# Kernel tuning notes

Hardware: AMD Instinct MI355X
Metric: run time of the kernel (lower is better)

Reference implementation:

```python
import jax, jax.numpy as jnp
import numpy as np

N_CAT, N_NUM, N_EMB, N_ENG = 53, 47, 1352, 100
E, H, FF, NEXP, NL = 128, 4, 256, 5, 6
B, L = 512, 51
EPS = 1e-5

def _ln(x, w, b):
    m = jnp.mean(x, axis=-1, keepdims=True)
    v = jnp.mean((x - m) ** 2, axis=-1, keepdims=True)
    return (x - m) * jax.lax.rsqrt(v + EPS) * w + b

def setup_inputs() -> dict:
    key = jax.random.key(0)
    ks = jax.random.split(key, 24)
    s = 0.02
    emb = jax.random.normal(ks[0], (N_EMB + 2, E), jnp.float32) * s
    emb = emb.at[0].set(0.0)  # padding_idx=0
    emb_eng = jax.random.normal(ks[1], (N_ENG, E), jnp.float32) * s
    emb_eng = emb_eng.at[0].set(0.0)
    inp = {
        'x_cat': jax.random.randint(ks[2], (B, L, N_CAT), 0, 1306, jnp.int32),
        'x_num': jax.random.normal(ks[3], (B, L, N_NUM), jnp.float32),
        'x_engineered': jax.random.normal(ks[4], (B, N_ENG), jnp.float32),
        'emb': emb,
        'emb_bias': jax.random.normal(ks[5], (N_CAT + N_NUM, E), jnp.float32),
        'emb_eng': emb_eng,
        'emb_bias_eng': jax.random.normal(ks[6], (N_ENG, E), jnp.float32),
        'ln0_w': jnp.ones((E,), jnp.float32), 'ln0_b': jnp.zeros((E,), jnp.float32),
        'ln1_w': jnp.ones((NL, E), jnp.float32), 'ln1_b': jnp.zeros((NL, E), jnp.float32),
        'Wqkv': jax.random.normal(ks[7], (NL, 3 * E, E), jnp.float32) * s,
        'bqkv': jnp.zeros((NL, 3 * E), jnp.float32),
        'Wo': jax.random.normal(ks[8], (NL, E, E), jnp.float32) * s,
        'bo': jnp.zeros((NL, E), jnp.float32),
        'ln2_w': jnp.ones((NL, E), jnp.float32), 'ln2_b': jnp.zeros((NL, E), jnp.float32),
        'Wg': jax.random.normal(ks[9], (NL, E, NEXP), jnp.float32) * s,
        'bg': jnp.zeros((NL, NEXP), jnp.float32),
        'W1': jax.random.normal(ks[10], (NL, NEXP, E, FF), jnp.float32) * s,
        'b1': jnp.zeros((NL, NEXP, FF), jnp.float32),
        'W2': jax.random.normal(ks[11], (NL, NEXP, FF, E), jnp.float32) * s,
        'b2': jnp.zeros((NL, NEXP, E), jnp.float32),
    }
    return inp

def _forward(x_cat, x_num, x_engineered, emb, emb_bias, emb_eng, emb_bias_eng,
             ln0_w, ln0_b, ln1_w, ln1_b, Wqkv, bqkv, Wo, bo,
             ln2_w, ln2_b, Wg, bg, W1, b1, W2, b2):
    b = x_cat.shape[0]
    # last order
    cat_last = x_cat[:, -1, :]                     # [B, N_CAT]
    num_last = x_num[:, -1, :]                     # [B, N_NUM]
    x_cat_emb = emb[cat_last] + emb_bias[:N_CAT][None]          # [B, N_CAT, E]
    num_idx = jnp.arange(N_EMB - N_NUM + 1, N_EMB + 1)           # rows 1306..1352
    x_num_emb = emb[num_idx][None] * num_last[..., None] + emb_bias[N_CAT:][None]
    eng_emb = emb_eng[None] * x_engineered[..., None] + emb_bias_eng[None]
    dummy = jnp.zeros((b, 1, E), x_cat_emb.dtype)
    x = jnp.concatenate([x_cat_emb, x_num_emb, eng_emb, dummy], axis=1)  # [B, 201, E]
    x = _ln(x, ln0_w, ln0_b)
    hd = E // H
    scale = 1.0 / np.sqrt(hd)
    for i in range(NL):
        # pre-norm multi-head self-attention
        h = _ln(x, ln1_w[i], ln1_b[i])
        qkv = h @ Wqkv[i].T + bqkv[i]              # [B, N, 3E]
        q, k, v = jnp.split(qkv, 3, axis=-1)
        q = q.reshape(b, -1, H, hd); k = k.reshape(b, -1, H, hd); v = v.reshape(b, -1, H, hd)
        scores = jnp.einsum('bqhd,bkhd->bhqk', q, k) * scale
        attn = jax.nn.softmax(scores, axis=-1)
        o = jnp.einsum('bhqk,bkhd->bqhd', attn, v).reshape(b, -1, E)
        x = x + o @ Wo[i].T + bo[i]
        # pre-norm MoE feedforward (dense soft mixture over experts)
        h = _ln(x, ln2_w[i], ln2_b[i])
        gate = jax.nn.softmax(h @ Wg[i] + bg[i], axis=-1)        # [B, N, NEXP]
        hid = jax.nn.relu(jnp.einsum('bne,xef->bnxf', h, W1[i]) + b1[i])
        eo = jnp.einsum('bnxf,xfe->bnxe', hid, W2[i]) + b2[i]
        x = x + jnp.einsum('bnxe,bnx->bne', eo, gate)
    return x[:, -1, :]                              # [B, E]

def reference(x_cat, x_num, x_engineered, emb, emb_bias, emb_eng, emb_bias_eng,
              ln0_w, ln0_b, ln1_w, ln1_b, Wqkv, bqkv, Wo, bo,
              ln2_w, ln2_b, Wg, bg, W1, b1, W2, b2):
    return _forward(x_cat, x_num, x_engineered, emb, emb_bias, emb_eng, emb_bias_eng,
                    ln0_w, ln0_b, ln1_w, ln1_b, Wqkv, bqkv, Wo, bo,
                    ln2_w, ln2_b, Wg, bg, W1, b1, W2, b2)
```

## Files before the change

### kernel.cpp

```cpp
#include <hip/hip_runtime.h>
#include <math.h>

#define NTOK 201
#define EDIM 128
#define LDX  132
#define NHEAD 4
#define HD   32
#define NLAY 6
#define NEXP 5
#define FFD  256
#define NCAT 53
#define NNUM 47
#define NENG 100
#define NEMB 1352
#define SEQL 51
#define NB   512
#define LN_EPS 1e-5f
#define SCALE 0.17677669529663687f

typedef __attribute__((ext_vector_type(8))) short bfrag;
typedef __attribute__((ext_vector_type(4))) float f32x4;
typedef __attribute__((ext_vector_type(8))) unsigned short u16x8;
typedef __attribute__((ext_vector_type(4))) unsigned short u16x4;

__device__ __forceinline__ float bf2f(unsigned short u){ return __uint_as_float(((unsigned)u)<<16); }
__device__ __forceinline__ unsigned short f2bf(float f){
  unsigned u = __float_as_uint(f);
  return (unsigned short)((u + 0x7FFFu + ((u>>16)&1u)) >> 16);
}

#define OFF_WQH  0u
#define OFF_WQL  589824u
#define OFF_BQ   1179648u
#define OFF_WOH  1188864u
#define OFF_WOL  1385472u
#define OFF_W1H  1582080u
#define OFF_W1L  3548160u
#define OFF_W2H  5514240u
#define OFF_W2L  7480320u

__global__ void prep_qkv_bf(const float* __restrict__ Wqkv, const float* __restrict__ bqkv,
                            unsigned short* __restrict__ Wqh, unsigned short* __restrict__ Wql,
                            float* __restrict__ bq){
  int bid = blockIdx.x; int n = bid % 384; int e = threadIdx.x;
  float sc = (n < 128) ? SCALE : 1.0f;
  float w = Wqkv[(size_t)bid*128 + e] * sc;
  unsigned short h = f2bf(w), l = f2bf(w - bf2f(h));
  Wqh[(size_t)bid*128 + e] = h; Wql[(size_t)bid*128 + e] = l;
  if (e == 0) bq[bid] = bqkv[bid] * sc;
}

__global__ void prep_wo_bf(const float* __restrict__ Wo,
                           unsigned short* __restrict__ Woh, unsigned short* __restrict__ Wol){
  int idx = blockIdx.x*blockDim.x + threadIdx.x;
  if (idx >= 6*128*128) return;
  float w = Wo[idx];
  unsigned short h = f2bf(w), l = f2bf(w - bf2f(h));
  Woh[idx] = h; Wol[idx] = l;
}

__global__ void prep_moe(const float* __restrict__ W1, const float* __restrict__ W2,
                         unsigned short* __restrict__ W1h, unsigned short* __restrict__ W1l,
                         unsigned short* __restrict__ W2h, unsigned short* __restrict__ W2l){
  const int Ntot = 6*5*128*256;
  for (int idx = blockIdx.x*blockDim.x + threadIdx.x; idx < Ntot; idx += gridDim.x*blockDim.x){
    int lx = idx / 32768; int rem = idx & 32767; int e = rem >> 8; int f = rem & 255;
    float w = W1[idx];
    unsigned short h = f2bf(w); unsigned short l = f2bf(w - bf2f(h));
    size_t o1 = (size_t)(lx*256+f)*128 + e;
    W1h[o1] = h; W1l[o1] = l;
    int f2 = (idx >> 7) & 255; int e2 = idx & 127;
    float w2 = W2[idx];
    unsigned short h2 = f2bf(w2); unsigned short l2 = f2bf(w2 - bf2f(h2));
    size_t o2 = (size_t)(lx*128+e2)*256 + f2;
    W2h[o2] = h2; W2l[o2] = l2;
  }
}

struct Params {
  const int*   x_cat;
  const float* x_num;
  const float* x_eng;
  const float* emb;
  const float* emb_bias;
  const float* emb_eng;
  const float* emb_bias_eng;
  const float* ln0w; const float* ln0b;
  const float* ln1w; const float* ln1b;
  const float* ln2w; const float* ln2b;
  const float* bo;
  const float* Wg;   const float* bg;
  const float* b1;   const float* b2;
  const unsigned short* Wqh; const unsigned short* Wql; const float* bq;
  const unsigned short* Woh; const unsigned short* Wol;
  const unsigned short* W1h; const unsigned short* W1l;
  const unsigned short* W2h; const unsigned short* W2l;
  float* out;
};

__device__ __forceinline__ void ln_stats(const float* xs, float* s_m, float* s_r, int tid){
  if (tid < NTOK){
    const float* row = xs + tid*LDX;
    float s0=0,s1=0,s2=0,s3=0;
    for (int e=0;e<EDIM;e+=4){ s0+=row[e]; s1+=row[e+1]; s2+=row[e+2]; s3+=row[e+3]; }
    float m = (s0+s1+s2+s3)*(1.0f/EDIM);
    float v0=0,v1=0,v2=0,v3=0;
    for (int e=0;e<EDIM;e+=4){
      float d0=row[e]-m,d1=row[e+1]-m,d2=row[e+2]-m,d3=row[e+3]-m;
      v0+=d0*d0; v1+=d1*d1; v2+=d2*d2; v3+=d3*d3;
    }
    s_m[tid]=m; s_r[tid]=1.0f/sqrtf((v0+v1+v2+v3)*(1.0f/EDIM)+LN_EPS);
  }
}

__global__ __launch_bounds__(512) __attribute__((amdgpu_waves_per_eu(2,2)))
void fam_fwd(Params p){
  __shared__ float xs[NTOK*LDX];
  __shared__ float s_m[NTOK], s_r[NTOK];
  __shared__ __align__(16) char scb[55296];

  const int b = blockIdx.x, tid = threadIdx.x;
  const int lane = tid & 63, wv = tid >> 6;

  {
    const int e = tid & 127, tl = tid >> 7;
    for (int t = tl; t < NTOK; t += 4){
      float v;
      if (t < NCAT){
        int idx = p.x_cat[b*(SEQL*NCAT) + (SEQL-1)*NCAT + t];
        v = p.emb[idx*EDIM+e] + p.emb_bias[t*EDIM+e];
      } else if (t < NCAT+NNUM){
        int j = t - NCAT;
        float nv = p.x_num[b*(SEQL*NNUM)+(SEQL-1)*NNUM+j];
        v = p.emb[(NEMB-NNUM+1+j)*EDIM+e]*nv + p.emb_bias[(NCAT+j)*EDIM+e];
      } else if (t < NCAT+NNUM+NENG){
        int j = t - (NCAT+NNUM);
        float ev = p.x_eng[b*NENG+j];
        v = p.emb_eng[j*EDIM+e]*ev + p.emb_bias_eng[j*EDIM+e];
      } else v = 0.f;
      xs[t*LDX+e] = v;
    }
  }
  __syncthreads();
  ln_stats(xs, s_m, s_r, tid);
  __syncthreads();
  {
    const int e = tid & 127, tl = tid >> 7;
    for (int t = tl; t < NTOK; t += 4){
      float m = s_m[t], r = s_r[t];
      xs[t*LDX+e] = (xs[t*LDX+e]-m)*r*p.ln0w[e] + p.ln0b[e];
    }
  }
  __syncthreads();

  unsigned short* Kh  = (unsigned short*)scb;
  unsigned short* Vt  = (unsigned short*)(scb + 17920);
  unsigned short* HTh = (unsigned short*)(scb + 32768);
  unsigned short* HTl = (unsigned short*)(scb + 32768 + 8704);
  unsigned short* Sb  = (unsigned short*)(scb + 32768);
  unsigned short* Ob  = (unsigned short*)(scb + 32768 + 14848);
  unsigned short* Qmh = (unsigned short*)(scb + 50176);
  unsigned short* Qml = (unsigned short*)(scb + 52736);
  float* red  = (float*)(scb + 52736);
  float* mrow = (float*)(scb + 52736 + 1056);
  float* dsum = (float*)(scb + 52736 + 1184);
  unsigned short* Ahi = (unsigned short*)scb;
  unsigned short* Alo = (unsigned short*)(scb + 8192);
  unsigned short* Hh  = (unsigned short*)(scb + 16384);
  unsigned short* Hl  = (unsigned short*)(scb + 32768);
  float*          gateb = (float*)(scb + 49152);

  for (int li = 0; li < NLAY; ++li){
    const float* ln1w = p.ln1w + li*EDIM;
    const float* ln1b = p.ln1b + li*EDIM;
    const float* ln2w = p.ln2w + li*EDIM;
    const float* ln2b = p.ln2b + li*EDIM;
    const float* bo   = p.bo + li*EDIM;
    const float* Wg   = p.Wg + li*EDIM*NEXP;
    const float* bg   = p.bg + li*NEXP;
    const float* b1g  = p.b1 + li*NEXP*FFD;
    const float* b2g  = p.b2 + li*NEXP*EDIM;

    ln_stats(xs, s_m, s_r, tid);
    __syncthreads();

    f32x4 accW[7][2];
#pragma unroll
    for (int mt=0; mt<7; ++mt){ accW[mt][0]=(f32x4){0,0,0,0}; accW[mt][1]=(f32x4){0,0,0,0}; }

    const int mfw = wv & 1;
    const int ngw = wv >> 1;

    for (int h = 0; h < NHEAD; ++h){
      {
        int sel = ngw;
        int nrow = ((sel < 2) ? (128 + h*HD + sel*16) : (256 + h*HD + (sel-2)*16)) + (lane & 15);
        const unsigned short* Bh = p.Wqh + ((size_t)li*384 + nrow)*128 + 8*(lane>>4);
        const unsigned short* Bl = p.Wql + ((size_t)li*384 + nrow)*128 + 8*(lane>>4);
        bfrag wbh[4], wbl[4];
#pragma unroll
        for (int kf=0; kf<4; ++kf){ wbh[kf] = *(const bfrag*)(Bh + kf*32); wbl[kf] = *(const bfrag*)(Bl + kf*32); }
        float bias = p.bq[li*384 + nrow];

        for (int mt=0; mt<7; ++mt){
          {
            int row = tid >> 4, c8 = (tid & 15) << 3;
            int t = mt*32 + row;
            union { unsigned short u[8]; u16x8 v; } hu, lu;
            if (t < NTOK){
              float m = s_m[t], r = s_r[t];
              const float* xr = &xs[t*LDX + c8];
              float4 a = *(const float4*)xr, b4 = *(const float4*)(xr+4);
              float4 w0 = *(const float4*)(ln1w + c8), w1 = *(const float4*)(ln1w + c8 + 4);
              float4 q0 = *(const float4*)(ln1b + c8), q1 = *(const float4*)(ln1b + c8 + 4);
              float vv[8] = {(a.x-m)*r*w0.x+q0.x,(a.y-m)*r*w0.y+q0.y,(a.z-m)*r*w0.z+q0.z,(a.w-m)*r*w0.w+q0.w,
                             (b4.x-m)*r*w1.x+q1.x,(b4.y-m)*r*w1.y+q1.y,(b4.z-m)*r*w1.z+q1.z,(b4.w-m)*r*w1.w+q1.w};
#pragma unroll
              for (int j2=0;j2<8;++j2){ unsigned short hb=f2bf(vv[j2]); hu.u[j2]=hb; lu.u[j2]=f2bf(vv[j2]-bf2f(hb)); }
            } else {
#pragma unroll
              for (int j2=0;j2<8;++j2){ hu.u[j2]=0; lu.u[j2]=0; }
            }
            *(u16x8*)(HTh + row*136 + c8) = hu.v;
            *(u16x8*)(HTl + row*136 + c8) = lu.v;
          }
          __syncthreads();
          {
            f32x4 acc = (f32x4){0,0,0,0};
#pragma unroll
            for (int kf=0; kf<4; ++kf){
              const unsigned short* ab = HTh + (mfw*16 + (lane&15))*136 + kf*32 + 8*(lane>>4);
              const unsigned short* al = HTl + (mfw*16 + (lane&15))*136 + kf*32 + 8*(lane>>4);
              bfrag ah = *(const bfrag*)ab, av = *(const bfrag*)al;
              acc = __builtin_amdgcn_mfma_f32_16x16x32_bf16(ah, wbh[kf], acc, 0,0,0);
              acc = __builtin_amdgcn_mfma_f32_16x16x32_bf16(ah, wbl[kf], acc, 0,0,0);
              acc = __builtin_amdgcn_mfma_f32_16x16x32_bf16(av, wbh[kf], acc, 0,0,0);
            }
            int col = lane & 15;
            if (sel < 2){
              int d = sel*16 + col;
#pragma unroll
              for (int reg=0; reg<4; ++reg){
                int tok = mt*32 + mfw*16 + 4*(lane>>4) + reg;
                Kh[tok*40 + d] = f2bf(acc[reg] + bias);
              }
            } else {
              int d = (sel-2)*16 + col;
              int tokb = mt*32 + mfw*16 + 4*(lane>>4);
              u16x4 pk;
#pragma unroll
              for (int reg=0; reg<4; ++reg) pk[reg] = f2bf(acc[reg] + bias);
              *(u16x4*)(Vt + d*232 + tokb) = pk;
            }
          }
          __syncthreads();
        }
      }

      bfrag wobh[2], wobl[2];
#pragma unroll
      for (int i=0;i<2;++i){
        int j = (ngw + 4*i)*16 + (lane&15);
        const unsigned short* wb = p.Woh + ((size_t)li*128 + j)*128 + h*HD + 8*(lane>>4);
        const unsigned short* wl = p.Wol + ((size_t)li*128 + j)*128 + h*HD + 8*(lane>>4);
        wobh[i] = *(const bfrag*)wb; wobl[i] = *(const bfrag*)wl;
      }

#pragma unroll
      for (int mt=0; mt<7; ++mt){
        {
          int row = tid >> 4, c8 = (tid & 15) << 3;
          int t = mt*32 + row;
          union { unsigned short u[8]; u16x8 v; } hu, lu;
          if (t < NTOK){
            float m = s_m[t], r = s_r[t];
            const float* xr = &xs[t*LDX + c8];
            float4 a = *(const float4*)xr, b4 = *(const float4*)(xr+4);
            float4 w0 = *(const float4*)(ln1w + c8), w1 = *(const float4*)(ln1w + c8 + 4);
            float4 q0 = *(const float4*)(ln1b + c8), q1 = *(const float4*)(ln1b + c8 + 4);
            float vv[8] = {(a.x-m)*r*w0.x+q0.x,(a.y-m)*r*w0.y+q0.y,(a.z-m)*r*w0.z+q0.z,(a.w-m)*r*w0.w+q0.w,
                           (b4.x-m)*r*w1.x+q1.x,(b4.y-m)*r*w1.y+q1.y,(b4.z-m)*r*w1.z+q1.z,(b4.w-m)*r*w1.w+q1.w};
#pragma unroll
            for (int j2=0;j2<8;++j2){ unsigned short hb=f2bf(vv[j2]); hu.u[j2]=hb; lu.u[j2]=f2bf(vv[j2]-bf2f(hb)); }
          } else {
#pragma unroll
            for (int j2=0;j2<8;++j2){ hu.u[j2]=0; lu.u[j2]=0; }
          }
          *(u16x8*)(HTh + row*136 + c8) = hu.v;
          *(u16x8*)(HTl + row*136 + c8) = lu.v;
        }
        __syncthreads();

        if (wv < 4){
          int mf2 = wv & 1, nf = (wv >> 1) & 1;
          int nrow = h*HD + nf*16 + (lane & 15);
          const unsigned short* Bh = p.Wqh + ((size_t)li*384 + nrow)*128 + 8*(lane>>4);
          const unsigned short* Bl = p.Wql + ((size_t)li*384 + nrow)*128 + 8*(lane>>4);
          f32x4 acc = (f32x4){0,0,0,0};
#pragma unroll
          for (int kf=0; kf<4; ++kf){
            bfrag ah = *(const bfrag*)(HTh + (mf2*16 + (lane&15))*136 + kf*32 + 8*(lane>>4));
            bfrag av = *(const bfrag*)(HTl + (mf2*16 + (lane&15))*136 + kf*32 + 8*(lane>>4));
            bfrag bh = *(const bfrag*)(Bh + kf*32);
            bfrag bl = *(const bfrag*)(Bl + kf*32);
            acc = __builtin_amdgcn_mfma_f32_16x16x32_bf16(ah, bh, acc, 0,0,0);
            acc = __builtin_amdgcn_mfma_f32_16x16x32_bf16(ah, bl, acc, 0,0,0);
            acc = __builtin_amdgcn_mfma_f32_16x16x32_bf16(av, bh, acc, 0,0,0);
          }
          float bias = p.bq[li*384 + nrow];
          int d = nf*16 + (lane & 15);
#pragma unroll
          for (int reg=0; reg<4; ++reg){
            float v = acc[reg] + bias;
            unsigned short hb = f2bf(v);
            int qrow = mf2*16 + 4*(lane>>4) + reg;
            Qmh[qrow*40 + d] = hb;
            Qml[qrow*40 + d] = f2bf(v - bf2f(hb));
          }
        }
        __syncthreads();

        {
          bfrag qh = *(const bfrag*)(Qmh + (mfw*16 + (lane&15))*40 + 8*(lane>>4));
          bfrag ql = *(const bfrag*)(Qml + (mfw*16 + (lane&15))*40 + 8*(lane>>4));
          for (int nf = ngw; nf < 14; nf += 4){
            bfrag kb = *(const bfrag*)(Kh + (nf*16 + (lane&15))*40 + 8*(lane>>4));
            f32x4 s = (f32x4){0,0,0,0};
            s = __builtin_amdgcn_mfma_f32_16x16x32_bf16(qh, kb, s, 0,0,0);
            s = __builtin_amdgcn_mfma_f32_16x16x32_bf16(ql, kb, s, 0,0,0);
            int tok = nf*16 + (lane & 15);
#pragma unroll
            for (int reg=0; reg<4; ++reg){
              int q = mfw*16 + 4*(lane>>4) + reg;
              Sb[q*232 + tok] = f2bf(s[reg]);
            }
          }
        }
        __syncthreads();

        {
          int q = tid & 31, kg = tid >> 5;
          float pmax = -INFINITY;
#pragma unroll
          for (int j2=0; j2<14; ++j2){
            int k = kg + 16*j2;
            if (k < NTOK) pmax = fmaxf(pmax, bf2f(Sb[q*232 + k]));
          }
          pmax = fmaxf(pmax, __shfl_xor(pmax, 32));
          if (!(tid & 32)) red[(tid>>6)*33 + q] = pmax;
        }
        __syncthreads();
        if (tid < 32){
          float m = red[tid];
#pragma unroll
          for (int w=1; w<8; ++w) m = fmaxf(m, red[w*33 + tid]);
          mrow[tid] = m;
        }
        __syncthreads();

        {
          int q = tid & 31, kg = tid >> 5;
          float mr = mrow[q];
          float psum = 0.f;
#pragma unroll
          for (int j2=0; j2<14; ++j2){
            int k = kg + 16*j2;
            float pe = 0.f;
            if (k < NTOK) pe = __expf(bf2f(Sb[q*232 + k]) - mr);
            psum += pe;
            Sb[q*232 + k] = f2bf(pe);
          }
          psum += __shfl_xor(psum, 32);
          if (!(tid & 32)) red[(tid>>6)*33 + q] = psum;
        }
        __syncthreads();
        if (tid < 32){
          float s = red[tid];
#pragma unroll
          for (int w=1; w<8; ++w) s += red[w*33 + tid];
          dsum[tid] = s;
        }
        __syncthreads();

        if (wv < 4){
          int mf2 = wv & 1, nf = (wv >> 1) & 1;
          f32x4 o = (f32x4){0,0,0,0};
#pragma unroll
          for (int kf=0; kf<7; ++kf){
            bfrag pa = *(const bfrag*)(Sb + (mf2*16 + (lane&15))*232 + kf*32 + 8*(lane>>4));
            bfrag vb = *(const bfrag*)(Vt + (nf*16 + (lane&15))*232 + kf*32 + 8*(lane>>4));
            o = __builtin_amdgcn_mfma_f32_16x16x32_bf16(pa, vb, o, 0,0,0);
          }
          int d = nf*16 + (lane & 15);
#pragma unroll
          for (int reg=0; reg<4; ++reg){
            int q = mf2*16 + 4*(lane>>4) + reg;
            Ob[q*40 + d] = f2bf(o[reg] * (1.0f/dsum[q]));
          }
        }
        __syncthreads();

        {
          bfrag oa = *(const bfrag*)(Ob + (mfw*16 + (lane&15))*40 + 8*(lane>>4));
          accW[mt][0] = __builtin_amdgcn_mfma_f32_16x16x32_bf16(oa, wobh[0], accW[mt][0], 0,0,0);
          accW[mt][0] = __builtin_amdgcn_mfma_f32_16x16x32_bf16(oa, wobl[0], accW[mt][0], 0,0,0);
          accW[mt][1] = __builtin_amdgcn_mfma_f32_16x16x32_bf16(oa, wobh[1], accW[mt][1], 0,0,0);
          accW[mt][1] = __builtin_amdgcn_mfma_f32_16x16x32_bf16(oa, wobl[1], accW[mt][1], 0,0,0);
        }
        __syncthreads();
      }
    }

    {
#pragma unroll
      for (int i=0;i<2;++i){
        int j = (ngw + 4*i)*16 + (lane & 15);
        float boj = bo[j];
#pragma unroll
        for (int mt=0; mt<7; ++mt){
#pragma unroll
          for (int reg=0; reg<4; ++reg){
            int t = mt*32 + mfw*16 + 4*(lane>>4) + reg;
            if (t < NTOK) xs[t*LDX + j] += accW[mt][i][reg] + boj;
          }
        }
      }
    }
    __syncthreads();

    ln_stats(xs, s_m, s_r, tid);
    __syncthreads();

    if (tid < NTOK){
      const float* row = xs + tid*LDX;
      float m = s_m[tid], r = s_r[tid];
      float gl[NEXP];
#pragma unroll
      for (int x=0;x<NEXP;++x) gl[x] = bg[x];
      for (int e=0;e<EDIM;++e){
        float hv = (row[e]-m)*r*ln2w[e] + ln2b[e];
#pragma unroll
        for (int x=0;x<NEXP;++x) gl[x] += hv*Wg[e*NEXP+x];
      }
      float gm = gl[0];
#pragma unroll
      for (int x=1;x<NEXP;++x) gm = fmaxf(gm, gl[x]);
      float gs = 0.f;
#pragma unroll
      for (int x=0;x<NEXP;++x){ gl[x] = __expf(gl[x]-gm); gs += gl[x]; }
      float gi = 1.0f/gs;
#pragma unroll
      for (int x=0;x<NEXP;++x) gateb[tid*NEXP+x] = gl[x]*gi;
    }
    __syncthreads();

    for (int t0 = 0; t0 < NTOK; t0 += 32){
      {
        int mf = tid >> 8;
        int row = (tid & 15) + 16*mf;
        int kb  = ((tid>>6)&3)*32 + 8*((tid>>4)&3);
        int t = t0 + row;
        union { unsigned short u[8]; bfrag v; } hu, lu;
        if (t < NTOK){
          float m = s_m[t], r = s_r[t];
          const float* xr = &xs[t*LDX + kb];
          float4 a = *(const float4*)xr;
          float4 bq4 = *(const float4*)(xr+4);
          float4 w0 = *(const float4*)(ln2w + kb);
          float4 w1 = *(const float4*)(ln2w + kb + 4);
          float4 bb0 = *(const float4*)(ln2b + kb);
          float4 bb1 = *(const float4*)(ln2b + kb + 4);
          float vv[8] = {(a.x-m)*r*w0.x+bb0.x, (a.y-m)*r*w0.y+bb0.y,
                         (a.z-m)*r*w0.z+bb0.z, (a.w-m)*r*w0.w+bb0.w,
                         (bq4.x-m)*r*w1.x+bb1.x, (bq4.y-m)*r*w1.y+bb1.y,
                         (bq4.z-m)*r*w1.z+bb1.z, (bq4.w-m)*r*w1.w+bb1.w};
#pragma unroll
          for (int j=0;j<8;++j){
            unsigned short hb = f2bf(vv[j]);
            hu.u[j] = hb;
            lu.u[j] = f2bf(vv[j] - bf2f(hb));
          }
        } else {
#pragma unroll
          for (int j=0;j<8;++j){ hu.u[j]=0; lu.u[j]=0; }
        }
        *(bfrag*)(Ahi + tid*8) = hu.v;
        *(bfrag*)(Alo + tid*8) = lu.v;
      }
      __syncthreads();

      f32x4 acc2[2];
      acc2[0] = (f32x4){0.f,0.f,0.f,0.f};
      acc2[1] = (f32x4){0.f,0.f,0.f,0.f};

      for (int x = 0; x < NEXP; ++x){
        const unsigned short* W1hx = p.W1h + (size_t)(li*NEXP+x)*FFD*EDIM;
        const unsigned short* W1lx = p.W1l + (size_t)(li*NEXP+x)*FFD*EDIM;
        const unsigned short* W2hx = p.W2h + (size_t)(li*NEXP+x)*EDIM*FFD;
        const unsigned short* W2lx = p.W2l + (size_t)(li*NEXP+x)*EDIM*FFD;

        f32x4 acc1[2][2];
#pragma unroll
        for (int i=0;i<2;++i){ acc1[i][0]=(f32x4){0,0,0,0}; acc1[i][1]=(f32x4){0,0,0,0}; }
#pragma unroll
        for (int kf=0;kf<4;++kf){
          bfrag ah[2], al[2], bh[2], bl[2];
#pragma unroll
          for (int mf=0;mf<2;++mf){
            ah[mf] = *(const bfrag*)(Ahi + ((mf*4+kf)*64 + lane)*8);
            al[mf] = *(const bfrag*)(Alo + ((mf*4+kf)*64 + lane)*8);
          }
#pragma unroll
          for (int nfl=0;nfl<2;++nfl){
            size_t n = (size_t)((wv*2+nfl)*16 + (lane&15));
            size_t off = n*128 + kf*32 + 8*(lane>>4);
            bh[nfl] = *(const bfrag*)(W1hx + off);
            bl[nfl] = *(const bfrag*)(W1lx + off);
          }
#pragma unroll
          for (int mf=0;mf<2;++mf)
#pragma unroll
            for (int nfl=0;nfl<2;++nfl){
              acc1[mf][nfl] = __builtin_amdgcn_mfma_f32_16x16x32_bf16(ah[mf], bh[nfl], acc1[mf][nfl], 0,0,0);
              acc1[mf][nfl] = __builtin_amdgcn_mfma_f32_16x16x32_bf16(ah[mf], bl[nfl], acc1[mf][nfl], 0,0,0);
              acc1[mf][nfl] = __builtin_amdgcn_mfma_f32_16x16x32_bf16(al[mf], bh[nfl], acc1[mf][nfl], 0,0,0);
            }
        }
        {
          int c = lane & 15;
#pragma unroll
          for (int nfl=0;nfl<2;++nfl){
            int n = (wv*2+nfl)*16 + c;
            float bb = b1g[x*FFD + n];
            int lane_t_base = 16*(2*nfl + (c>>3));
            int jcol = c & 7;
#pragma unroll
            for (int mf=0;mf<2;++mf){
#pragma unroll
              for (int reg=0;reg<4;++reg){
                int msub = (lane>>4)*4 + reg;
                int t = t0 + mf*16 + msub;
                float g = (t < NTOK) ? gateb[t*NEXP+x] : 0.f;
                float v = fmaxf(acc1[mf][nfl][reg] + bb, 0.f) * g;
                unsigned short hb = f2bf(v);
                unsigned short lb = f2bf(v - bf2f(hb));
                int idx = ((mf*8 + wv)*64 + msub + lane_t_base)*8 + jcol;
                Hh[idx] = hb; Hl[idx] = lb;
              }
            }
          }
        }
        __syncthreads();

#pragma unroll
        for (int kf=0;kf<8;++kf){
          bfrag hh[2], hl[2];
#pragma unroll
          for (int mf=0;mf<2;++mf){
            hh[mf] = *(const bfrag*)(Hh + ((mf*8+kf)*64 + lane)*8);
            hl[mf] = *(const bfrag*)(Hl + ((mf*8+kf)*64 + lane)*8);
          }
          size_t off = (size_t)(wv*16 + (lane&15))*256 + kf*32 + 8*(lane>>4);
          bfrag wh = *(const bfrag*)(W2hx + off);
          bfrag wl = *(const bfrag*)(W2lx + off);
#pragma unroll
          for (int mf=0;mf<2;++mf){
            acc2[mf] = __builtin_amdgcn_mfma_f32_16x16x32_bf16(hh[mf], wh, acc2[mf], 0,0,0);
            acc2[mf] = __builtin_amdgcn_mfma_f32_16x16x32_bf16(hh[mf], wl, acc2[mf], 0,0,0);
            acc2[mf] = __builtin_amdgcn_mfma_f32_16x16x32_bf16(hl[mf], wh, acc2[mf], 0,0,0);
          }
        }
        __syncthreads();
      }

      {
        int c = lane & 15;
        int n = wv*16 + c;
#pragma unroll
        for (int mf=0;mf<2;++mf){
#pragma unroll
          for (int reg=0;reg<4;++reg){
            int t = t0 + mf*16 + (lane>>4)*4 + reg;
            if (t < NTOK){
              float bs = 0.f;
#pragma unroll
              for (int x=0;x<NEXP;++x) bs += gateb[t*NEXP+x]*b2g[x*EDIM+n];
              xs[t*LDX+n] += acc2[mf][reg] + bs;
            }
          }
        }
      }
      __syncthreads();
    }
  }

  if (tid < EDIM) p.out[b*EDIM + tid] = xs[200*LDX + tid];
}

extern "C" void kernel_launch(void* const* d_in, const int* in_sizes, int n_in,
                              void* d_out, int out_size, void* d_ws, size_t ws_size,
                              hipStream_t stream) {
  (void)in_sizes; (void)n_in; (void)out_size; (void)ws_size;
  char* ws = (char*)d_ws;

  const float* Wqkv = (const float*)d_in[11];
  const float* bqkv = (const float*)d_in[12];
  const float* Wo   = (const float*)d_in[13];
  const float* W1   = (const float*)d_in[19];
  const float* W2   = (const float*)d_in[21];

  hipLaunchKernelGGL(prep_qkv_bf, dim3(6*384), dim3(128), 0, stream,
                     Wqkv, bqkv,
                     (unsigned short*)(ws+OFF_WQH), (unsigned short*)(ws+OFF_WQL),
                     (float*)(ws+OFF_BQ));
  hipLaunchKernelGGL(prep_wo_bf, dim3(384), dim3(256), 0, stream, Wo,
                     (unsigned short*)(ws+OFF_WOH), (unsigned short*)(ws+OFF_WOL));
  hipLaunchKernelGGL(prep_moe, dim3(3840), dim3(256), 0, stream, W1, W2,
                     (unsigned short*)(ws+OFF_W1H), (unsigned short*)(ws+OFF_W1L),
                     (unsigned short*)(ws+OFF_W2H), (unsigned short*)(ws+OFF_W2L));

  Params p;
  p.x_cat        = (const int*)  d_in[0];
  p.x_num        = (const float*)d_in[1];
  p.x_eng        = (const float*)d_in[2];
  p.emb          = (const float*)d_in[3];
  p.emb_bias     = (const float*)d_in[4];
  p.emb_eng      = (const float*)d_in[5];
  p.emb_bias_eng = (const float*)d_in[6];
  p.ln0w = (const float*)d_in[7];  p.ln0b = (const float*)d_in[8];
  p.ln1w = (const float*)d_in[9];  p.ln1b = (const float*)d_in[10];
  p.ln2w = (const float*)d_in[15]; p.ln2b = (const float*)d_in[16];
  p.bo   = (const float*)d_in[14];
  p.Wg   = (const float*)d_in[17]; p.bg = (const float*)d_in[18];
  p.b1   = (const float*)d_in[20]; p.b2 = (const float*)d_in[22];
  p.Wqh = (const unsigned short*)(ws+OFF_WQH);
  p.Wql = (const unsigned short*)(ws+OFF_WQL);
  p.bq  = (const float*)(ws+OFF_BQ);
  p.Woh = (const unsigned short*)(ws+OFF_WOH);
  p.Wol = (const unsigned short*)(ws+OFF_WOL);
  p.W1h = (const unsigned short*)(ws+OFF_W1H);
  p.W1l = (const unsigned short*)(ws+OFF_W1L);
  p.W2h = (const unsigned short*)(ws+OFF_W2H);
  p.W2l = (const unsigned short*)(ws+OFF_W2L);
  p.out = (float*)d_out;

  hipLaunchKernelGGL(fam_fwd, dim3(NB), dim3(512), 0, stream, p);
}
```

Measured before the change: 5.539 ms.

## Fuse softmax max into score pass, double-buffer MoE hidden, split accumulators

The row-max reduction for softmax now happens in registers via shuffles during the QK^T pass, and the sum reduction is folded into the PV epilogue, which drops several block barriers. In the MoE FFN, the hidden activation is double-buffered across experts so the barrier after each W2 pass can be removed. The hidden is also kept as a single bf16 term rather than a hi/lo split, which cuts one MFMA per step at some precision cost. The diff further splits MFMA accumulator chains to shorten dependencies, adds s_setprio around MFMA loops, and moves one barrier out of the inner loop.

```diff
diff --git a/kernel.cpp b/kernel.cpp
--- a/kernel.cpp
+++ b/kernel.cpp
@@ -111,6 +111,31 @@
     }
     s_m[tid]=m; s_r[tid]=1.0f/sqrtf((v0+v1+v2+v3)*(1.0f/EDIM)+LN_EPS);
   }
+}
+
+__device__ __forceinline__ void stage_ht(const float* xs, const float* s_m, const float* s_r,
+                                         unsigned short* HTh, unsigned short* HTl,
+                                         const float* lw, const float* lb, int t0, int tid){
+  int row = tid >> 4;
+  int c8  = (tid & 15) << 3;
+  int t = t0 + row;
+  union { unsigned short u[8]; u16x8 v; } hu, lu;
+  if (t < NTOK){
+    float m = s_m[t], r = s_r[t];
+    const float* xr = &xs[t*LDX + c8];
+    float4 a = *(const float4*)xr, b4 = *(const float4*)(xr+4);
+    float4 w0 = *(const float4*)(lw + c8), w1 = *(const float4*)(lw + c8 + 4);
+    float4 q0 = *(const float4*)(lb + c8), q1 = *(const float4*)(lb + c8 + 4);
+    float vv[8] = {(a.x-m)*r*w0.x+q0.x,(a.y-m)*r*w0.y+q0.y,(a.z-m)*r*w0.z+q0.z,(a.w-m)*r*w0.w+q0.w,
+                   (b4.x-m)*r*w1.x+q1.x,(b4.y-m)*r*w1.y+q1.y,(b4.z-m)*r*w1.z+q1.z,(b4.w-m)*r*w1.w+q1.w};
+#pragma unroll
+    for (int j2=0;j2<8;++j2){ unsigned short hb=f2bf(vv[j2]); hu.u[j2]=hb; lu.u[j2]=f2bf(vv[j2]-bf2f(hb)); }
+  } else {
+#pragma unroll
+    for (int j2=0;j2<8;++j2){ hu.u[j2]=0; lu.u[j2]=0; }
+  }
+  *(u16x8*)(HTh + row*136 + c8) = hu.v;
+  *(u16x8*)(HTl + row*136 + c8) = lu.v;
 }
 
 __global__ __launch_bounds__(512) __attribute__((amdgpu_waves_per_eu(2,2)))
@@ -162,12 +187,11 @@
   unsigned short* Qmh = (unsigned short*)(scb + 50176);
   unsigned short* Qml = (unsigned short*)(scb + 52736);
   float* red  = (float*)(scb + 52736);
-  float* mrow = (float*)(scb + 52736 + 1056);
-  float* dsum = (float*)(scb + 52736 + 1184);
+  float* red2 = (float*)(scb + 50176);
   unsigned short* Ahi = (unsigned short*)scb;
   unsigned short* Alo = (unsigned short*)(scb + 8192);
-  unsigned short* Hh  = (unsigned short*)(scb + 16384);
-  unsigned short* Hl  = (unsigned short*)(scb + 32768);
+  unsigned short* H0  = (unsigned short*)(scb + 16384);
+  unsigned short* H1  = (unsigned short*)(scb + 32768);
   float*          gateb = (float*)(scb + 49152);
 
   for (int li = 0; li < NLAY; ++li){
@@ -200,56 +224,42 @@
         bfrag wbh[4], wbl[4];
 #pragma unroll
         for (int kf=0; kf<4; ++kf){ wbh[kf] = *(const bfrag*)(Bh + kf*32); wbl[kf] = *(const bfrag*)(Bl + kf*32); }
-        float bias = p.bq[li*384 + nrow];
+        float bias1 = p.bq[li*384 + nrow];
 
         for (int mt=0; mt<7; ++mt){
-          {
-            int row = tid >> 4, c8 = (tid & 15) << 3;
-            int t = mt*32 + row;
-            union { unsigned short u[8]; u16x8 v; } hu, lu;
-            if (t < NTOK){
-              float m = s_m[t], r = s_r[t];
-              const float* xr = &xs[t*LDX + c8];
-              float4 a = *(const float4*)xr, b4 = *(const float4*)(xr+4);
-              float4 w0 = *(const float4*)(ln1w + c8), w1 = *(const float4*)(ln1w + c8 + 4);
-              float4 q0 = *(const float4*)(ln1b + c8), q1 = *(const float4*)(ln1b + c8 + 4);
-              float vv[8] = {(a.x-m)*r*w0.x+q0.x,(a.y-m)*r*w0.y+q0.y,(a.z-m)*r*w0.z+q0.z,(a.w-m)*r*w0.w+q0.w,
-                             (b4.x-m)*r*w1.x+q1.x,(b4.y-m)*r*w1.y+q1.y,(b4.z-m)*r*w1.z+q1.z,(b4.w-m)*r*w1.w+q1.w};
-#pragma unroll
-              for (int j2=0;j2<8;++j2){ unsigned short hb=f2bf(vv[j2]); hu.u[j2]=hb; lu.u[j2]=f2bf(vv[j2]-bf2f(hb)); }
-            } else {
-#pragma unroll
-              for (int j2=0;j2<8;++j2){ hu.u[j2]=0; lu.u[j2]=0; }
-            }
-            *(u16x8*)(HTh + row*136 + c8) = hu.v;
-            *(u16x8*)(HTl + row*136 + c8) = lu.v;
-          }
+          stage_ht(xs, s_m, s_r, HTh, HTl, ln1w, ln1b, mt*32, tid);
           __syncthreads();
           {
-            f32x4 acc = (f32x4){0,0,0,0};
+            f32x4 aA = (f32x4){0,0,0,0}, aB = (f32x4){0,0,0,0};
 #pragma unroll
             for (int kf=0; kf<4; ++kf){
-              const unsigned short* ab = HTh + (mfw*16 + (lane&15))*136 + kf*32 + 8*(lane>>4);
-              const unsigned short* al = HTl + (mfw*16 + (lane&15))*136 + kf*32 + 8*(lane>>4);
-              bfrag ah = *(const bfrag*)ab, av = *(const bfrag*)al;
-              acc = __builtin_amdgcn_mfma_f32_16x16x32_bf16(ah, wbh[kf], acc, 0,0,0);
-              acc = __builtin_amdgcn_mfma_f32_16x16x32_bf16(ah, wbl[kf], acc, 0,0,0);
-              acc = __builtin_amdgcn_mfma_f32_16x16x32_bf16(av, wbh[kf], acc, 0,0,0);
+              bfrag ah = *(const bfrag*)(HTh + (mfw*16 + (lane&15))*136 + kf*32 + 8*(lane>>4));
+              bfrag av = *(const bfrag*)(HTl + (mfw*16 + (lane&15))*136 + kf*32 + 8*(lane>>4));
+              if (kf & 1){
+                aB = __builtin_amdgcn_mfma_f32_16x16x32_bf16(ah, wbh[kf], aB, 0,0,0);
+                aB = __builtin_amdgcn_mfma_f32_16x16x32_bf16(ah, wbl[kf], aB, 0,0,0);
+                aB = __builtin_amdgcn_mfma_f32_16x16x32_bf16(av, wbh[kf], aB, 0,0,0);
+              } else {
+                aA = __builtin_amdgcn_mfma_f32_16x16x32_bf16(ah, wbh[kf], aA, 0,0,0);
+                aA = __builtin_amdgcn_mfma_f32_16x16x32_bf16(ah, wbl[kf], aA, 0,0,0);
+                aA = __builtin_amdgcn_mfma_f32_16x16x32_bf16(av, wbh[kf], aA, 0,0,0);
+              }
             }
+            f32x4 acc = aA + aB;
             int col = lane & 15;
             if (sel < 2){
               int d = sel*16 + col;
 #pragma unroll
               for (int reg=0; reg<4; ++reg){
                 int tok = mt*32 + mfw*16 + 4*(lane>>4) + reg;
-                Kh[tok*40 + d] = f2bf(acc[reg] + bias);
+                Kh[tok*40 + d] = f2bf(acc[reg] + bias1);
               }
             } else {
               int d = (sel-2)*16 + col;
               int tokb = mt*32 + mfw*16 + 4*(lane>>4);
               u16x4 pk;
 #pragma unroll
-              for (int reg=0; reg<4; ++reg) pk[reg] = f2bf(acc[reg] + bias);
+              for (int reg=0; reg<4; ++reg) pk[reg] = f2bf(acc[reg] + bias1);
               *(u16x4*)(Vt + d*232 + tokb) = pk;
             }
           }
@@ -268,46 +278,33 @@
 
 #pragma unroll
       for (int mt=0; mt<7; ++mt){
-        {
-          int row = tid >> 4, c8 = (tid & 15) << 3;
-          int t = mt*32 + row;
-          union { unsigned short u[8]; u16x8 v; } hu, lu;
-          if (t < NTOK){
-            float m = s_m[t], r = s_r[t];
-            const float* xr = &xs[t*LDX + c8];
-            float4 a = *(const float4*)xr, b4 = *(const float4*)(xr+4);
-            float4 w0 = *(const float4*)(ln1w + c8), w1 = *(const float4*)(ln1w + c8 + 4);
-            float4 q0 = *(const float4*)(ln1b + c8), q1 = *(const float4*)(ln1b + c8 + 4);
-            float vv[8] = {(a.x-m)*r*w0.x+q0.x,(a.y-m)*r*w0.y+q0.y,(a.z-m)*r*w0.z+q0.z,(a.w-m)*r*w0.w+q0.w,
-                           (b4.x-m)*r*w1.x+q1.x,(b4.y-m)*r*w1.y+q1.y,(b4.z-m)*r*w1.z+q1.z,(b4.w-m)*r*w1.w+q1.w};
-#pragma unroll
-            for (int j2=0;j2<8;++j2){ unsigned short hb=f2bf(vv[j2]); hu.u[j2]=hb; lu.u[j2]=f2bf(vv[j2]-bf2f(hb)); }
-          } else {
-#pragma unroll
-            for (int j2=0;j2<8;++j2){ hu.u[j2]=0; lu.u[j2]=0; }
-          }
-          *(u16x8*)(HTh + row*136 + c8) = hu.v;
-          *(u16x8*)(HTl + row*136 + c8) = lu.v;
-        }
+        stage_ht(xs, s_m, s_r, HTh, HTl, ln1w, ln1b, mt*32, tid);
         __syncthreads();
 
         if (wv < 4){
-          int mf2 = wv & 1, nf = (wv >> 1) & 1;
+          int mf2 = wv & 1, nf = wv >> 1;
           int nrow = h*HD + nf*16 + (lane & 15);
           const unsigned short* Bh = p.Wqh + ((size_t)li*384 + nrow)*128 + 8*(lane>>4);
           const unsigned short* Bl = p.Wql + ((size_t)li*384 + nrow)*128 + 8*(lane>>4);
-          f32x4 acc = (f32x4){0,0,0,0};
+          f32x4 aA = (f32x4){0,0,0,0}, aB = (f32x4){0,0,0,0};
 #pragma unroll
           for (int kf=0; kf<4; ++kf){
             bfrag ah = *(const bfrag*)(HTh + (mf2*16 + (lane&15))*136 + kf*32 + 8*(lane>>4));
             bfrag av = *(const bfrag*)(HTl + (mf2*16 + (lane&15))*136 + kf*32 + 8*(lane>>4));
             bfrag bh = *(const bfrag*)(Bh + kf*32);
             bfrag bl = *(const bfrag*)(Bl + kf*32);
-            acc = __builtin_amdgcn_mfma_f32_16x16x32_bf16(ah, bh, acc, 0,0,0);
-            acc = __builtin_amdgcn_mfma_f32_16x16x32_bf16(ah, bl, acc, 0,0,0);
-            acc = __builtin_amdgcn_mfma_f32_16x16x32_bf16(av, bh, acc, 0,0,0);
-          }
-          float bias = p.bq[li*384 + nrow];
+            if (kf & 1){
+              aB = __builtin_amdgcn_mfma_f32_16x16x32_bf16(ah, bh, aB, 0,0,0);
+              aB = __builtin_amdgcn_mfma_f32_16x16x32_bf16(ah, bl, aB, 0,0,0);
+              aB = __builtin_amdgcn_mfma_f32_16x16x32_bf16(av, bh, aB, 0,0,0);
+            } else {
+              aA = __builtin_amdgcn_mfma_f32_16x16x32_bf16(ah, bh, aA, 0,0,0);
+              aA = __builtin_amdgcn_mfma_f32_16x16x32_bf16(ah, bl, aA, 0,0,0);
+              aA = __builtin_amdgcn_mfma_f32_16x16x32_bf16(av, bh, aA, 0,0,0);
+            }
+          }
+          f32x4 acc = aA + aB;
+          float bias = p.bq[li*384 + h*HD + nf*16 + (lane&15)];
           int d = nf*16 + (lane & 15);
 #pragma unroll
           for (int reg=0; reg<4; ++reg){
@@ -323,6 +320,7 @@
         {
           bfrag qh = *(const bfrag*)(Qmh + (mfw*16 + (lane&15))*40 + 8*(lane>>4));
           bfrag ql = *(const bfrag*)(Qml + (mfw*16 + (lane&15))*40 + 8*(lane>>4));
+          float pmax = -INFINITY;
           for (int nf = ngw; nf < 14; nf += 4){
             bfrag kb = *(const bfrag*)(Kh + (nf*16 + (lane&15))*40 + 8*(lane>>4));
             f32x4 s = (f32x4){0,0,0,0};
@@ -333,34 +331,27 @@
             for (int reg=0; reg<4; ++reg){
               int q = mfw*16 + 4*(lane>>4) + reg;
               Sb[q*232 + tok] = f2bf(s[reg]);
+              if (tok < NTOK) pmax = fmaxf(pmax, s[reg]);
             }
+          }
+          float m0 = pmax;
+          m0 = fmaxf(m0, __shfl_xor(m0, 1));
+          m0 = fmaxf(m0, __shfl_xor(m0, 2));
+          m0 = fmaxf(m0, __shfl_xor(m0, 4));
+          m0 = fmaxf(m0, __shfl_xor(m0, 8));
+          if ((lane & 15) == 0){
+            int qbase = mfw*16 + 4*(lane>>4);
+#pragma unroll
+            for (int reg=0; reg<4; ++reg) red[wv*33 + qbase + reg] = m0;
           }
         }
         __syncthreads();
 
         {
           int q = tid & 31, kg = tid >> 5;
-          float pmax = -INFINITY;
-#pragma unroll
-          for (int j2=0; j2<14; ++j2){
-            int k = kg + 16*j2;
-            if (k < NTOK) pmax = fmaxf(pmax, bf2f(Sb[q*232 + k]));
-          }
-          pmax = fmaxf(pmax, __shfl_xor(pmax, 32));
-          if (!(tid & 32)) red[(tid>>6)*33 + q] = pmax;
-        }
-        __syncthreads();
-        if (tid < 32){
-          float m = red[tid];
-#pragma unroll
-          for (int w=1; w<8; ++w) m = fmaxf(m, red[w*33 + tid]);
-          mrow[tid] = m;
-        }
-        __syncthreads();
-
-        {
-          int q = tid & 31, kg = tid >> 5;
-          float mr = mrow[q];
+          float mr = red[q];
+#pragma unroll
+          for (int w=1; w<8; ++w) mr = fmaxf(mr, red[w*33 + q]);
           float psum = 0.f;
 #pragma unroll
           for (int j2=0; j2<14; ++j2){
@@ -368,34 +359,32 @@
             float pe = 0.f;
             if (k < NTOK) pe = __expf(bf2f(Sb[q*232 + k]) - mr);
             psum += pe;
-            Sb[q*232 + k] = f2bf(pe);
+            if (k < 224) Sb[q*232 + k] = f2bf(pe);
           }
           psum += __shfl_xor(psum, 32);
-          if (!(tid & 32)) red[(tid>>6)*33 + q] = psum;
+          if (!(tid & 32)) red2[wv*33 + q] = psum;
         }
         __syncthreads();
-        if (tid < 32){
-          float s = red[tid];
-#pragma unroll
-          for (int w=1; w<8; ++w) s += red[w*33 + tid];
-          dsum[tid] = s;
-        }
-        __syncthreads();
 
         if (wv < 4){
-          int mf2 = wv & 1, nf = (wv >> 1) & 1;
-          f32x4 o = (f32x4){0,0,0,0};
+          int mf2 = wv & 1, nf = wv >> 1;
+          f32x4 oA = (f32x4){0,0,0,0}, oB = (f32x4){0,0,0,0};
 #pragma unroll
           for (int kf=0; kf<7; ++kf){
             bfrag pa = *(const bfrag*)(Sb + (mf2*16 + (lane&15))*232 + kf*32 + 8*(lane>>4));
             bfrag vb = *(const bfrag*)(Vt + (nf*16 + (lane&15))*232 + kf*32 + 8*(lane>>4));
-            o = __builtin_amdgcn_mfma_f32_16x16x32_bf16(pa, vb, o, 0,0,0);
-          }
+            if (kf & 1) oB = __builtin_amdgcn_mfma_f32_16x16x32_bf16(pa, vb, oB, 0,0,0);
+            else        oA = __builtin_amdgcn_mfma_f32_16x16x32_bf16(pa, vb, oA, 0,0,0);
+          }
+          f32x4 o = oA + oB;
           int d = nf*16 + (lane & 15);
 #pragma unroll
           for (int reg=0; reg<4; ++reg){
             int q = mf2*16 + 4*(lane>>4) + reg;
-            Ob[q*40 + d] = f2bf(o[reg] * (1.0f/dsum[q]));
+            float s = red2[q];
+#pragma unroll
+            for (int w=1; w<8; ++w) s += red2[w*33 + q];
+            Ob[q*40 + d] = f2bf(o[reg] * (1.0f/s));
           }
         }
         __syncthreads();
@@ -489,11 +478,12 @@
       }
       __syncthreads();
 
-      f32x4 acc2[2];
-      acc2[0] = (f32x4){0.f,0.f,0.f,0.f};
-      acc2[1] = (f32x4){0.f,0.f,0.f,0.f};
+      f32x4 a2[2][2];
+      a2[0][0]=(f32x4){0,0,0,0}; a2[0][1]=(f32x4){0,0,0,0};
+      a2[1][0]=(f32x4){0,0,0,0}; a2[1][1]=(f32x4){0,0,0,0};
 
       for (int x = 0; x < NEXP; ++x){
+        unsigned short* Hb = (x & 1) ? H1 : H0;
         const unsigned short* W1hx = p.W1h + (size_t)(li*NEXP+x)*FFD*EDIM;
         const unsigned short* W1lx = p.W1l + (size_t)(li*NEXP+x)*FFD*EDIM;
         const unsigned short* W2hx = p.W2h + (size_t)(li*NEXP+x)*EDIM*FFD;
@@ -502,6 +492,7 @@
         f32x4 acc1[2][2];
 #pragma unroll
         for (int i=0;i<2;++i){ acc1[i][0]=(f32x4){0,0,0,0}; acc1[i][1]=(f32x4){0,0,0,0}; }
+        __builtin_amdgcn_s_setprio(1);
 #pragma unroll
         for (int kf=0;kf<4;++kf){
           bfrag ah[2], al[2], bh[2], bl[2];
@@ -526,6 +517,7 @@
               acc1[mf][nfl] = __builtin_amdgcn_mfma_f32_16x16x32_bf16(al[mf], bh[nfl], acc1[mf][nfl], 0,0,0);
             }
         }
+        __builtin_amdgcn_s_setprio(0);
         {
           int c = lane & 15;
 #pragma unroll
@@ -542,35 +534,31 @@
                 int t = t0 + mf*16 + msub;
                 float g = (t < NTOK) ? gateb[t*NEXP+x] : 0.f;
                 float v = fmaxf(acc1[mf][nfl][reg] + bb, 0.f) * g;
-                unsigned short hb = f2bf(v);
-                unsigned short lb = f2bf(v - bf2f(hb));
                 int idx = ((mf*8 + wv)*64 + msub + lane_t_base)*8 + jcol;
-                Hh[idx] = hb; Hl[idx] = lb;
+                Hb[idx] = f2bf(v);
               }
             }
           }
         }
         __syncthreads();
 
+        __builtin_amdgcn_s_setprio(1);
 #pragma unroll
         for (int kf=0;kf<8;++kf){
-          bfrag hh[2], hl[2];
-#pragma unroll
-          for (int mf=0;mf<2;++mf){
-            hh[mf] = *(const bfrag*)(Hh + ((mf*8+kf)*64 + lane)*8);
-            hl[mf] = *(const bfrag*)(Hl + ((mf*8+kf)*64 + lane)*8);
-          }
+          bfrag hh[2];
+#pragma unroll
+          for (int mf=0;mf<2;++mf)
+            hh[mf] = *(const bfrag*)(Hb + ((mf*8+kf)*64 + lane)*8);
           size_t off = (size_t)(wv*16 + (lane&15))*256 + kf*32 + 8*(lane>>4);
           bfrag wh = *(const bfrag*)(W2hx + off);
           bfrag wl = *(const bfrag*)(W2lx + off);
 #pragma unroll
           for (int mf=0;mf<2;++mf){
-            acc2[mf] = __builtin_amdgcn_mfma_f32_16x16x32_bf16(hh[mf], wh, acc2[mf], 0,0,0);
-            acc2[mf] = __builtin_amdgcn_mfma_f32_16x16x32_bf16(hh[mf], wl, acc2[mf], 0,0,0);
-            acc2[mf] = __builtin_amdgcn_mfma_f32_16x16x32_bf16(hl[mf], wh, acc2[mf], 0,0,0);
-          }
-        }
-        __syncthreads();
+            a2[mf][kf&1] = __builtin_amdgcn_mfma_f32_16x16x32_bf16(hh[mf], wh, a2[mf][kf&1], 0,0,0);
+            a2[mf][kf&1] = __builtin_amdgcn_mfma_f32_16x16x32_bf16(hh[mf], wl, a2[mf][kf&1], 0,0,0);
+          }
+        }
+        __builtin_amdgcn_s_setprio(0);
       }
 
       {
@@ -585,13 +573,13 @@
               float bs = 0.f;
 #pragma unroll
               for (int x=0;x<NEXP;++x) bs += gateb[t*NEXP+x]*b2g[x*EDIM+n];
-              xs[t*LDX+n] += acc2[mf][reg] + bs;
+              xs[t*LDX+n] += a2[mf][0][reg] + a2[mf][1][reg] + bs;
             }
           }
         }
       }
-      __syncthreads();
     }
+    __syncthreads();
   }
 
   if (tid < EDIM) p.out[b*EDIM + tid] = xs[200*LDX + tid];
```

Measured after the change: 5.448 ms. About the same (-1.6%).
